# Kernel tuning notes

Hardware: AMD Instinct MI355X
Metric: run time of the kernel (lower is better)

## Reference

```python
import jax, jax.numpy as jnp
import numpy as np

K = 16
D = 1024
B = 65536

# Row-major off-diagonal index order matching the torch double loop (i, j, i != j)
_ii, _jj = np.nonzero(~np.eye(K, dtype=bool))  # each (K*(K-1),), row-major
OFF_I = jnp.asarray(_ii)
OFF_J = jnp.asarray(_jj)
DIAG = jnp.arange(K)


def setup_inputs() -> dict:
    key = jax.random.key(0)
    k1, k2, k3, k4, k5 = jax.random.split(key, 5)
    scale_d = 1.0 / np.sqrt(D)
    return {
        "x": jax.random.normal(k1, (B, D), dtype=jnp.float32),
        "Wd": jax.random.normal(k2, (K, D), dtype=jnp.float32) * scale_d,
        "bd": jax.random.normal(k3, (K,), dtype=jnp.float32) * 0.1,
        "Wo": jax.random.normal(k4, (K * (K - 1), D), dtype=jnp.float32) * scale_d,
        "bo": jax.random.normal(k5, (K * (K - 1),), dtype=jnp.float32) * 0.1 - 3.0,
    }


def reference(x, Wd, bd, Wo, bo):
    # Diagonal gates: (B, K)
    c_diag = jax.nn.sigmoid(jnp.einsum("bd,kd->bk", x, Wd) + bd)
    # Off-diagonal values: (B, K*(K-1)), non-positive
    off_vals = -jax.nn.softplus(jnp.einsum("bd,kd->bk", x, Wo) + bo)
    C = jnp.zeros((x.shape[0], K, K), dtype=x.dtype)
    C = C.at[:, OFF_I, OFF_J].set(off_vals)
    C = C.at[:, DIAG, DIAG].set(c_diag)
    return C
```

## Files before the change

kernel.cpp:

```cpp
#include <hip/hip_runtime.h>
#include <hip/hip_bf16.h>
#include <stdint.h>


typedef __bf16 bf16x8 __attribute__((ext_vector_type(8)));
typedef float f32x4 __attribute__((ext_vector_type(4)));

#define THREADS 256
#define BM 64
#define KSTEPS 32
#define WIMG 16384
#define WBYTES (WIMG * KSTEPS)

__device__ __forceinline__ unsigned bf_rtne(unsigned u) {
  return (u + 0x7fffu + ((u >> 16) & 1u)) >> 16;
}
__device__ __forceinline__ unsigned pack2(float lo, float hi) {
  return bf_rtne(__float_as_uint(lo)) | (bf_rtne(__float_as_uint(hi)) << 16);
}

__device__ __forceinline__ void gload_lds16(const void* g, void* l) {
  __builtin_amdgcn_global_load_lds(
      (const __attribute__((address_space(1))) unsigned int*)g,
      (__attribute__((address_space(3))) unsigned int*)l, 16, 0, 0);
}

__global__ void prep_kernel(const float* __restrict__ Wd, const float* __restrict__ bd,
                            const float* __restrict__ Wo, const float* __restrict__ bo,
                            char* __restrict__ wbuf, float* __restrict__ bias) {
  const int c = blockIdx.x;
  const int t = threadIdx.x;
  const int i = c >> 4, j = c & 15;
  const float* src;
  float b;
  if (i == j) { src = Wd + i * 1024; b = bd[i]; }
  else { int r = i * 15 + (j < i ? j : j - 1); src = Wo + r * 1024; b = bo[r]; }
  if (t == 0) bias[c] = b;
  const int kk = t * 4;
  const int img = kk >> 5, k5 = kk & 31;
  float4 v = *reinterpret_cast<const float4*>(src + kk);
  uint2 h;
  h.x = pack2(v.x, v.y);
  h.y = pack2(v.z, v.w);
  const unsigned off = (unsigned)((c * 64 + k5 * 2) ^ (((c >> 1) & 3) << 4));
  *reinterpret_cast<uint2*>(wbuf + img * WIMG + off) = h;
}

__global__ __launch_bounds__(THREADS, 4) void cap_main(
    const float* __restrict__ x, const char* __restrict__ wbuf,
    const float* __restrict__ bias, float* __restrict__ out) {
  __shared__ char smem[40960];

  const int tid = threadIdx.x;
  const int wid = tid >> 6;
  const int lane = tid & 63;
  const int l15 = lane & 15;
  const int l4 = lane >> 4;

  const size_t blkRow = (size_t)blockIdx.x * BM;

  const int ar = tid >> 2;
  const int akc = tid & 3;
  const float* xs = x + (blkRow + (size_t)ar) * 1024 + akc * 8;
  const unsigned awz = (unsigned)((ar * 64 + akc * 16) ^ (((ar >> 1) & 3) << 4));

  const unsigned sw = (unsigned)(((l15 >> 1) & 3) << 4);
  const unsigned abase = (unsigned)((l15 * 64 + l4 * 16) ^ sw);
  const unsigned bbase = (unsigned)(((wid * 64 + l15) * 64 + l4 * 16) ^ sw);

  f32x4 acc[4][4];
#pragma unroll
  for (int m = 0; m < 4; ++m)
#pragma unroll
    for (int n = 0; n < 4; ++n) acc[m][n] = (f32x4){0.f, 0.f, 0.f, 0.f};

  {
    float4 p0 = *reinterpret_cast<const float4*>(xs);
    float4 p1 = *reinterpret_cast<const float4*>(xs + 4);
#pragma unroll
    for (int i = 0; i < 4; ++i)
      gload_lds16(wbuf + (wid * 4 + i) * 1024 + lane * 16,
                  smem + 8192 + (wid * 4 + i) * 1024);
    uint4 w;
    w.x = pack2(p0.x, p0.y); w.y = pack2(p0.z, p0.w);
    w.z = pack2(p1.x, p1.y); w.w = pack2(p1.z, p1.w);
    *reinterpret_cast<uint4*>(smem + awz) = w;
  }
  __syncthreads();

  for (int t = 0; t < KSTEPS; ++t) {
    const int cur = t & 1;
    const char* Ac = smem + cur * 4096;
    const char* Bc = smem + 8192 + cur * 16384;
    char* An = smem + (cur ^ 1) * 4096;
    char* Bn = smem + 8192 + (cur ^ 1) * 16384;

    float4 p0, p1;
    if (t + 1 < KSTEPS) {
      const float* xsp = xs + (t + 1) * 32;
      p0 = *reinterpret_cast<const float4*>(xsp);
      p1 = *reinterpret_cast<const float4*>(xsp + 4);
      const char* wsp = wbuf + (t + 1) * WIMG;
#pragma unroll
      for (int i = 0; i < 4; ++i)
        gload_lds16(wsp + (wid * 4 + i) * 1024 + lane * 16, Bn + (wid * 4 + i) * 1024);
    }

    bf16x8 af[4], bfr[4];
#pragma unroll
    for (int m = 0; m < 4; ++m)
      af[m] = *reinterpret_cast<const bf16x8*>(Ac + abase + m * 1024);
#pragma unroll
    for (int n = 0; n < 4; ++n)
      bfr[n] = *reinterpret_cast<const bf16x8*>(Bc + bbase + n * 1024);
#pragma unroll
    for (int m = 0; m < 4; ++m)
#pragma unroll
      for (int n = 0; n < 4; ++n)
        acc[m][n] = __builtin_amdgcn_mfma_f32_16x16x32_bf16(af[m], bfr[n], acc[m][n], 0, 0, 0);

    if (t + 1 < KSTEPS) {
      uint4 w;
      w.x = pack2(p0.x, p0.y); w.y = pack2(p0.z, p0.w);
      w.z = pack2(p1.x, p1.y); w.w = pack2(p1.z, p1.w);
      *reinterpret_cast<uint4*>(An + awz) = w;
    }
    __syncthreads();
  }

  float bs[4];
#pragma unroll
  for (int n = 0; n < 4; ++n) bs[n] = bias[wid * 64 + n * 16 + l15];

  const int rr2 = tid >> 4;
  const int co = (tid & 15) * 16;
  const char* rdp = smem + rr2 * 1040 + co * 4;

#pragma unroll
  for (int p = 0; p < 4; ++p) {
#pragma unroll
    for (int n = 0; n < 4; ++n) {
      const int col = wid * 64 + n * 16 + l15;
      const bool diag = (col % 17) == 0;
#pragma unroll
      for (int j2 = 0; j2 < 4; ++j2) {
        const int rr = l4 * 4 + j2;
        float v = acc[p][n][j2] + bs[n];
        float e = __expf(-fabsf(v));
        float sig = (v >= 0.f) ? 1.f / (1.f + e) : e / (1.f + e);
        float sp = fmaxf(v, 0.f) + __logf(1.f + e);
        *reinterpret_cast<float*>(smem + rr * 1040 + col * 4) = diag ? sig : -sp;
      }
    }
    __syncthreads();
    float4 o0 = *reinterpret_cast<const float4*>(rdp);
    float4 o1 = *reinterpret_cast<const float4*>(rdp + 16);
    float4 o2 = *reinterpret_cast<const float4*>(rdp + 32);
    float4 o3 = *reinterpret_cast<const float4*>(rdp + 48);
    float* orow = out + (blkRow + (size_t)(p * 16 + rr2)) * 256 + co;
    *reinterpret_cast<float4*>(orow) = o0;
    *reinterpret_cast<float4*>(orow + 4) = o1;
    *reinterpret_cast<float4*>(orow + 8) = o2;
    *reinterpret_cast<float4*>(orow + 12) = o3;
    __syncthreads();
  }
}

extern "C" void kernel_launch(void* const* d_in, const int* in_sizes, int n_in,
                              void* d_out, int out_size, void* d_ws, size_t ws_size,
                              hipStream_t stream) {
  const float* x = (const float*)d_in[0];
  const float* Wd = (const float*)d_in[1];
  const float* bd = (const float*)d_in[2];
  const float* Wo = (const float*)d_in[3];
  const float* bo = (const float*)d_in[4];
  float* out = (float*)d_out;
  char* wbuf = (char*)d_ws;
  float* bias = (float*)(wbuf + WBYTES);

  prep_kernel<<<dim3(256), dim3(256), 0, stream>>>(Wd, bd, Wo, bo, wbuf, bias);
  cap_main<<<dim3(1024), dim3(THREADS), 0, stream>>>(x, wbuf, bias, out);
}
```

Before: 106.7 us.

## Triple-buffer A and B via direct global-to-LDS loads with vmcnt-gated barriers

Loads x tiles as fp32 straight into LDS with global_load_lds, using an XOR swizzle, instead of staging them through registers and converting before the store. The bf16 conversion moves to fragment-read time. A three-slot ring for both A and B, with s_waitcnt vmcnt(6) plus barrier, keeps two chunks in flight to hide global latency. In exchange, shared memory grows to 72 KB, the occupancy hint drops from 4 to 2 blocks, LDS read traffic for A doubles, and some loads are redundant at the tail.

```diff
diff --git a/kernel.cpp b/kernel.cpp
--- a/kernel.cpp
+++ b/kernel.cpp
@@ -12,13 +12,23 @@
 #define WIMG 16384
 #define WBYTES (WIMG * KSTEPS)
 
+#define ASLOT 8192
+#define BBASE 24576
+#define BSLOT 16384
+#define SMEM_SZ 73728
+
 __device__ __forceinline__ unsigned bf_rtne(unsigned u) {
   return (u + 0x7fffu + ((u >> 16) & 1u)) >> 16;
 }
 __device__ __forceinline__ unsigned pack2(float lo, float hi) {
   return bf_rtne(__float_as_uint(lo)) | (bf_rtne(__float_as_uint(hi)) << 16);
 }
-
+__device__ __forceinline__ bf16x8 packfrag(const f32x4& a, const f32x4& b) {
+  uint4 u;
+  u.x = pack2(a[0], a[1]); u.y = pack2(a[2], a[3]);
+  u.z = pack2(b[0], b[1]); u.w = pack2(b[2], b[3]);
+  return *reinterpret_cast<bf16x8*>(&u);
+}
 __device__ __forceinline__ void gload_lds16(const void* g, void* l) {
   __builtin_amdgcn_global_load_lds(
       (const __attribute__((address_space(1))) unsigned int*)g,
@@ -46,27 +56,29 @@
   *reinterpret_cast<uint2*>(wbuf + img * WIMG + off) = h;
 }
 
-__global__ __launch_bounds__(THREADS, 4) void cap_main(
+__global__ __launch_bounds__(THREADS, 2) void cap_main(
     const float* __restrict__ x, const char* __restrict__ wbuf,
     const float* __restrict__ bias, float* __restrict__ out) {
-  __shared__ char smem[40960];
+  __shared__ char smem[SMEM_SZ];
 
   const int tid = threadIdx.x;
   const int wid = tid >> 6;
   const int lane = tid & 63;
   const int l15 = lane & 15;
   const int l4 = lane >> 4;
+  const int l7 = lane & 7;
+  const int l3 = lane >> 3;
 
   const size_t blkRow = (size_t)blockIdx.x * BM;
 
-  const int ar = tid >> 2;
-  const int akc = tid & 3;
-  const float* xs = x + (blkRow + (size_t)ar) * 1024 + akc * 8;
-  const unsigned awz = (unsigned)((ar * 64 + akc * 16) ^ (((ar >> 1) & 3) << 4));
+  const float* asrc0 = x + (blkRow + (size_t)((wid * 2 + 0) * 8 + l3)) * 1024 + ((l7 * 4) ^ (l3 << 2));
+  const float* asrc1 = x + (blkRow + (size_t)((wid * 2 + 1) * 8 + l3)) * 1024 + ((l7 * 4) ^ (l3 << 2));
+  const unsigned adst0 = (unsigned)((wid * 2 + 0) * 1024 + lane * 16);
+  const unsigned adst1 = (unsigned)((wid * 2 + 1) * 1024 + lane * 16);
 
-  const unsigned sw = (unsigned)(((l15 >> 1) & 3) << 4);
-  const unsigned abase = (unsigned)((l15 * 64 + l4 * 16) ^ sw);
-  const unsigned bbase = (unsigned)(((wid * 64 + l15) * 64 + l4 * 16) ^ sw);
+  const unsigned swA = (unsigned)((l15 & 7) << 4);
+  const unsigned swB = (unsigned)(((l15 >> 1) & 3) << 4);
+  const unsigned bbase = (unsigned)(((wid * 64 + l15) * 64 + l4 * 16) ^ swB);
 
   f32x4 acc[4][4];
 #pragma unroll
@@ -74,59 +86,58 @@
 #pragma unroll
     for (int n = 0; n < 4; ++n) acc[m][n] = (f32x4){0.f, 0.f, 0.f, 0.f};
 
-  {
-    float4 p0 = *reinterpret_cast<const float4*>(xs);
-    float4 p1 = *reinterpret_cast<const float4*>(xs + 4);
-#pragma unroll
-    for (int i = 0; i < 4; ++i)
-      gload_lds16(wbuf + (wid * 4 + i) * 1024 + lane * 16,
-                  smem + 8192 + (wid * 4 + i) * 1024);
-    uint4 w;
-    w.x = pack2(p0.x, p0.y); w.y = pack2(p0.z, p0.w);
-    w.z = pack2(p1.x, p1.y); w.w = pack2(p1.z, p1.w);
-    *reinterpret_cast<uint4*>(smem + awz) = w;
+#define STAGE(CH, ASL, BSL)                                                     \
+  {                                                                             \
+    gload_lds16(asrc0 + (CH) * 32, smem + (ASL) + adst0);                       \
+    gload_lds16(asrc1 + (CH) * 32, smem + (ASL) + adst1);                       \
+    const char* wsp = wbuf + (CH) * WIMG;                                       \
+    _Pragma("unroll") for (int i = 0; i < 4; ++i)                               \
+        gload_lds16(wsp + (wid * 4 + i) * 1024 + lane * 16,                     \
+                    smem + (BSL) + (wid * 4 + i) * 1024 + lane * 16);           \
   }
-  __syncthreads();
+
+  STAGE(0, 0, BBASE);
+  STAGE(1, ASLOT, BBASE + BSLOT);
+  asm volatile("s_waitcnt vmcnt(6)\n\ts_barrier" ::: "memory");
+
+  unsigned aR = 0, bR = BBASE;
+  unsigned aI = 2 * ASLOT, bI = BBASE + 2 * BSLOT;
 
   for (int t = 0; t < KSTEPS; ++t) {
-    const int cur = t & 1;
-    const char* Ac = smem + cur * 4096;
-    const char* Bc = smem + 8192 + cur * 16384;
-    char* An = smem + (cur ^ 1) * 4096;
-    char* Bn = smem + 8192 + (cur ^ 1) * 16384;
+    const int ch = (t + 2 < KSTEPS) ? t + 2 : KSTEPS - 1;
+    STAGE(ch, aI, bI);
 
-    float4 p0, p1;
-    if (t + 1 < KSTEPS) {
-      const float* xsp = xs + (t + 1) * 32;
-      p0 = *reinterpret_cast<const float4*>(xsp);
-      p1 = *reinterpret_cast<const float4*>(xsp + 4);
-      const char* wsp = wbuf + (t + 1) * WIMG;
-#pragma unroll
-      for (int i = 0; i < 4; ++i)
-        gload_lds16(wsp + (wid * 4 + i) * 1024 + lane * 16, Bn + (wid * 4 + i) * 1024);
-    }
-
+    const char* Ac = smem + aR;
+    const char* Bc = smem + bR;
     bf16x8 af[4], bfr[4];
 #pragma unroll
-    for (int m = 0; m < 4; ++m)
-      af[m] = *reinterpret_cast<const bf16x8*>(Ac + abase + m * 1024);
+    for (int m = 0; m < 4; ++m) {
+      const unsigned rb = (unsigned)((m * 16 + l15) * 128);
+      f32x4 u0 = *reinterpret_cast<const f32x4*>(Ac + rb + ((l4 * 32) ^ swA));
+      f32x4 u1 = *reinterpret_cast<const f32x4*>(Ac + rb + ((l4 * 32 + 16) ^ swA));
+      af[m] = packfrag(u0, u1);
+    }
 #pragma unroll
     for (int n = 0; n < 4; ++n)
       bfr[n] = *reinterpret_cast<const bf16x8*>(Bc + bbase + n * 1024);
+
 #pragma unroll
     for (int m = 0; m < 4; ++m)
 #pragma unroll
       for (int n = 0; n < 4; ++n)
         acc[m][n] = __builtin_amdgcn_mfma_f32_16x16x32_bf16(af[m], bfr[n], acc[m][n], 0, 0, 0);
 
-    if (t + 1 < KSTEPS) {
-      uint4 w;
-      w.x = pack2(p0.x, p0.y); w.y = pack2(p0.z, p0.w);
-      w.z = pack2(p1.x, p1.y); w.w = pack2(p1.z, p1.w);
-      *reinterpret_cast<uint4*>(An + awz) = w;
-    }
-    __syncthreads();
+    asm volatile("s_waitcnt vmcnt(6)\n\ts_barrier" ::: "memory");
+
+    aR = (aR == 2 * ASLOT) ? 0u : aR + ASLOT;
+    aI = (aI == 2 * ASLOT) ? 0u : aI + ASLOT;
+    bR = (bR == BBASE + 2 * BSLOT) ? (unsigned)BBASE : bR + BSLOT;
+    bI = (bI == BBASE + 2 * BSLOT) ? (unsigned)BBASE : bI + BSLOT;
   }
+#undef STAGE
+
+  asm volatile("s_waitcnt vmcnt(0)" ::: "memory");
+  __syncthreads();
 
   float bs[4];
 #pragma unroll
```

New measurement: 106.6 us. Within noise of the previous version (-0.1%).
